# Kernel optimization log

Measured on AMD Instinct MI355X. Metric: run time of the kernel, lower is better.

The kernel has to match this reference:

```python
import jax, jax.numpy as jnp
import numpy as np

B, T, HID = 1, 2048, 2048
H = 16            # num_heads == num_key_value_heads
D = HID // H      # head_dim == feature_dim == 128
EPS = 1e-5


def _layer_norm(x, eps=1e-5):
    mu = jnp.mean(x, axis=-1, keepdims=True)
    var = jnp.mean((x - mu) ** 2, axis=-1, keepdims=True)
    return (x - mu) * jax.lax.rsqrt(var + eps)


def _feature_map(x, gamma, beta):
    # ReBased feature map, flatten=False (parallel mode): affine then LayerNorm
    return _layer_norm(x * gamma + beta)


def setup_inputs() -> dict:
    key = jax.random.key(0)
    ks = jax.random.split(key, 8)
    s = HID ** -0.5
    return {
        "hidden_states": jax.random.normal(ks[0], (B, T, HID), jnp.float32),
        "Wq": jax.random.normal(ks[1], (HID, HID), jnp.float32) * s,
        "Wk": jax.random.normal(ks[2], (HID, HID), jnp.float32) * s,
        "Wv": jax.random.normal(ks[3], (HID, HID), jnp.float32) * s,
        "Wo": jax.random.normal(ks[4], (HID, HID), jnp.float32) * s,
        "gamma": 1.0 + 0.1 * jax.random.normal(ks[5], (D,), jnp.float32),
        "beta": 0.1 * jax.random.normal(ks[6], (D,), jnp.float32),
    }


def reference(hidden_states, Wq, Wk, Wv, Wo, gamma, beta):
    b, t, _ = hidden_states.shape
    # projections (nn.Linear: x @ W.T), split into heads: [b, t, h, d]
    q = (hidden_states @ Wq.T).reshape(b, t, H, D)
    k = (hidden_states @ Wk.T).reshape(b, t, H, D)
    v = (hidden_states @ Wv.T).reshape(b, t, H, D)
    # ReBased feature map (no quadratic flatten in parallel mode)
    q = _feature_map(q, gamma, beta)
    k = _feature_map(k, gamma, beta)
    # parallel_rebased: scale q, quadratic score, causal mask, normalize
    q = q * (D ** -0.5)
    attn = jnp.einsum('bqhd,bkhd->bhqk', q, k) ** 2  # (q.k)^2
    mask = jnp.tril(jnp.ones((t, t), dtype=bool))
    attn = jnp.where(mask, attn, 0.0)
    o = jnp.einsum('bhqk,bkhd->bqhd', attn, v)       # [b, t, h, d]
    z = jnp.sum(attn, axis=-1)                       # [b, h, t]
    o = o / (jnp.swapaxes(z, 1, 2)[..., None] + EPS)
    o = o.reshape(b, t, H * D)
    return o @ Wo.T
```

## Files before the change

kernel.cpp:

```cpp
#include <hip/hip_runtime.h>
#include <hip/hip_bf16.h>
#include <stdint.h>

typedef __bf16 bf16;
typedef __bf16 v8bf __attribute__((ext_vector_type(8)));
typedef __bf16 v4bf __attribute__((ext_vector_type(4)));
typedef float  v4f  __attribute__((ext_vector_type(4)));

#define TSEQ   2048
#define HIDDIM 2048
#define NHEAD  16
#define HDIM   128

__device__ __forceinline__ void async16(void* lds, const void* g)
{
    __builtin_amdgcn_global_load_lds(
        (__attribute__((address_space(1))) void*)(uintptr_t)g,
        (__attribute__((address_space(3))) void*)(unsigned int)(uintptr_t)lds,
        16, 0, 0);
}

__global__ __launch_bounds__(256) void conv5(const float* __restrict__ s0, bf16* __restrict__ d0,
                                             const float* __restrict__ s1, bf16* __restrict__ d1,
                                             const float* __restrict__ s2, bf16* __restrict__ d2,
                                             const float* __restrict__ s3, bf16* __restrict__ d3,
                                             const float* __restrict__ s4, bf16* __restrict__ d4)
{
    const float* src; bf16* dst;
    switch (blockIdx.y) {
        case 0: src = s0; dst = d0; break;
        case 1: src = s1; dst = d1; break;
        case 2: src = s2; dst = d2; break;
        case 3: src = s3; dst = d3; break;
        default: src = s4; dst = d4; break;
    }
    const size_t i = ((size_t)blockIdx.x * 256 + threadIdx.x) * 8;
    const float4 a = *(const float4*)(src + i);
    const float4 b = *(const float4*)(src + i + 4);
    v8bf o;
    o[0] = (bf16)a.x; o[1] = (bf16)a.y; o[2] = (bf16)a.z; o[3] = (bf16)a.w;
    o[4] = (bf16)b.x; o[5] = (bf16)b.y; o[6] = (bf16)b.z; o[7] = (bf16)b.w;
    *(v8bf*)(dst + i) = o;
}


#define PBAR() do { __builtin_amdgcn_sched_barrier(0); __builtin_amdgcn_s_barrier(); \
                    __builtin_amdgcn_sched_barrier(0); } while (0)

#define STU(ldst, gsrc) do { \
    async16((ldst) + w*512,        (gsrc) + (size_t)(w*8 + (l>>3))*2048); \
    async16((ldst) + 4096 + w*512, (gsrc) + (size_t)(64 + w*8 + (l>>3))*2048); \
} while (0)

#define RDA(buf) do { _Pragma("unroll") \
    for (int mi_ = 0; mi_ < 4; ++mi_) { \
        const bf16* p_ = &sA[(buf)*8192 + (wm*64 + mi_*16 + lr)*64]; \
        a[mi_][0] = *(const v8bf*)(p_ + c0); \
        a[mi_][1] = *(const v8bf*)(p_ + c1); } } while (0)

#define RDB(buf, nh) do { _Pragma("unroll") \
    for (int nj_ = 0; nj_ < 2; ++nj_) { \
        const bf16* p_ = &sB[(buf)*24576 + ((nh)*128 + wn*32 + nj_*16 + lr)*64]; \
        b[nj_][0] = *(const v8bf*)(p_ + c0); \
        b[nj_][1] = *(const v8bf*)(p_ + c1); } } while (0)

#define MQ(nh) do { _Pragma("unroll") \
    for (int mi_ = 0; mi_ < 4; ++mi_) { _Pragma("unroll") \
        for (int nj_ = 0; nj_ < 2; ++nj_) { \
            acc[mi_][(nh)*2+nj_] = __builtin_amdgcn_mfma_f32_16x16x32_bf16( \
                a[mi_][0], b[nj_][0], acc[mi_][(nh)*2+nj_], 0, 0, 0); \
            acc[mi_][(nh)*2+nj_] = __builtin_amdgcn_mfma_f32_16x16x32_bf16( \
                a[mi_][1], b[nj_][1], acc[mi_][(nh)*2+nj_], 0, 0, 0); \
        } } } while (0)

#define VMC(n) asm volatile("s_waitcnt vmcnt(" #n ")" ::: "memory")

__global__ __launch_bounds__(512, 2) void gemm_qkv384(const bf16* __restrict__ A,
    const bf16* __restrict__ Wcat, bf16* __restrict__ qb, bf16* __restrict__ kb,
    bf16* __restrict__ vt, const float* __restrict__ gamma, const float* __restrict__ beta)
{
    __shared__ __attribute__((aligned(16))) bf16 sA[2*8192];
    __shared__ __attribute__((aligned(16))) bf16 sB[2*24576];
    const int n0g = blockIdx.x * 384;
    const int m0  = blockIdx.y * 128;

    const int tid = threadIdx.x, l = tid & 63, w = tid >> 6;
    const int wm = w >> 2, wn = w & 3;
    const int quad = l >> 4, lr = l & 15;
    const int scol = ((l & 7) ^ ((l >> 3) & 7)) * 8;
    const int c0 = ((quad    ) ^ (lr & 7)) * 8;
    const int c1 = ((quad + 4) ^ (lr & 7)) * 8;

    const bf16* Ag = A    + (size_t)m0  * 2048 + scol;
    const bf16* Bg = Wcat + (size_t)n0g * 2048 + scol;

    v4f  acc[4][6] = {};
    v8bf a[4][2], b[2][2];

    STU(&sA[0],           Ag);
    STU(&sB[0],           Bg);
    STU(&sB[8192],        Bg + (size_t)128*2048);
    STU(&sB[16384],       Bg + (size_t)256*2048);
    STU(&sA[8192],        Ag + 64);
    STU(&sB[24576],       Bg + 64);
    STU(&sB[24576+8192],  Bg + (size_t)128*2048 + 64);
    VMC(10);
    __builtin_amdgcn_s_barrier();
    __builtin_amdgcn_sched_barrier(0);

#pragma unroll 1
    for (int it = 0; it < 16; ++it) {
        const int k1 =  it*128 + 64;
        const int k2 = (it*128 + 128) & 2047;
        const int k3 = (it*128 + 192) & 2047;

        RDA(0); RDB(0, 0);
        STU(&sB[24576+16384], Bg + (size_t)256*2048 + k1);
        PBAR(); __builtin_amdgcn_s_setprio(1); MQ(0); __builtin_amdgcn_s_setprio(0);
        VMC(10); PBAR();
        RDB(0, 1);
        STU(&sA[0], Ag + k2);
        STU(&sB[0], Bg + k2);
        PBAR(); __builtin_amdgcn_s_setprio(1); MQ(1); __builtin_amdgcn_s_setprio(0);
        VMC(12); PBAR();
        RDB(0, 2);
        STU(&sB[8192], Bg + (size_t)128*2048 + k2);
        PBAR(); __builtin_amdgcn_s_setprio(1); MQ(2); __builtin_amdgcn_s_setprio(0);
        VMC(10); PBAR();
        RDA(1); RDB(1, 0);
        STU(&sB[16384], Bg + (size_t)256*2048 + k2);
        PBAR(); __builtin_amdgcn_s_setprio(1); MQ(0); __builtin_amdgcn_s_setprio(0);
        VMC(10); PBAR();
        RDB(1, 1);
        STU(&sA[8192],  Ag + k3);
        STU(&sB[24576], Bg + k3);
        PBAR(); __builtin_amdgcn_s_setprio(1); MQ(1); __builtin_amdgcn_s_setprio(0);
        VMC(12); PBAR();
        RDB(1, 2);
        STU(&sB[24576+8192], Bg + (size_t)128*2048 + k3);
        PBAR(); __builtin_amdgcn_s_setprio(1); MQ(2); __builtin_amdgcn_s_setprio(0);
        VMC(10); PBAR();
    }
    VMC(0);
    __syncthreads();

    bf16* sT = sB;
    const int erow = tid >> 2;
    const int ecol = (tid & 3) * 32;
    float gv[32], bv[32];
#pragma unroll
    for (int i = 0; i < 8; ++i) {
        *(float4*)&gv[i*4] = *(const float4*)(gamma + ecol + i*4);
        *(float4*)&bv[i*4] = *(const float4*)(beta  + ecol + i*4);
    }

#pragma unroll
    for (int nh = 0; nh < 3; ++nh) {
        const int colg0 = n0g + nh*128;
        const int which = colg0 >> 11;
        if (which == 2) {
#pragma unroll
            for (int mi = 0; mi < 4; ++mi) {
                const int row = m0 + wm*64 + mi*16 + quad*4;
#pragma unroll
                for (int jj = 0; jj < 2; ++jj) {
                    const int c = (colg0 & 2047) + wn*32 + jj*16 + lr;
                    v4bf pk;
#pragma unroll
                    for (int r = 0; r < 4; ++r) pk[r] = (bf16)acc[mi][nh*2+jj][r];
                    *(v4bf*)(vt + (size_t)c*2048 + row) = pk;
                }
            }
        } else {
#pragma unroll
            for (int mi = 0; mi < 4; ++mi) {
                const int row = wm*64 + mi*16 + quad*4;
#pragma unroll
                for (int jj = 0; jj < 2; ++jj) {
                    const int col = wn*32 + jj*16 + lr;
#pragma unroll
                    for (int r = 0; r < 4; ++r)
                        sT[(row + r)*136 + col] = (bf16)acc[mi][nh*2+jj][r];
                }
            }
            __syncthreads();
            float x[32];
            float s = 0.f, q = 0.f;
#pragma unroll
            for (int i = 0; i < 4; ++i) {
                const v8bf v = *(const v8bf*)&sT[erow*136 + ecol + i*8];
#pragma unroll
                for (int k = 0; k < 8; ++k) {
                    const float xv = (float)v[k] * gv[i*8+k] + bv[i*8+k];
                    x[i*8+k] = xv; s += xv; q += xv*xv;
                }
            }
            s += __shfl_xor(s, 1); q += __shfl_xor(q, 1);
            s += __shfl_xor(s, 2); q += __shfl_xor(q, 2);
            const float mu = s * (1.0f/128.0f);
            float var = q * (1.0f/128.0f) - mu*mu;
            var = fmaxf(var, 0.0f);
            bf16* Cb = (which == 0) ? qb : kb;
            const float qs = (which == 0) ? 0.08838834764831845f : 1.0f;
            const float rstd = rsqrtf(var + 1e-5f) * qs;
            bf16* dst = Cb + (size_t)(m0 + erow)*2048 + (colg0 & 2047) + ecol;
#pragma unroll
            for (int i = 0; i < 4; ++i) {
                v8bf o;
#pragma unroll
                for (int k = 0; k < 8; ++k)
                    o[k] = (bf16)((x[i*8+k] - mu) * rstd);
                *(v8bf*)(dst + i*8) = o;
            }
            __syncthreads();
        }
    }
}


#define RDO(aa, bb, buf) do { _Pragma("unroll") \
    for (int mi_ = 0; mi_ < 4; ++mi_) { \
        const bf16* p_ = &sA[(buf)*8192 + (wm*64 + mi_*16 + lr)*64]; \
        aa[mi_][0] = *(const v8bf*)(p_ + c0); \
        aa[mi_][1] = *(const v8bf*)(p_ + c1); } \
    _Pragma("unroll") \
    for (int nj_ = 0; nj_ < 2; ++nj_) { \
        const bf16* p_ = &sB[(buf)*8192 + (wn*32 + nj_*16 + lr)*64]; \
        bb[nj_][0] = *(const v8bf*)(p_ + c0); \
        bb[nj_][1] = *(const v8bf*)(p_ + c1); } } while (0)

#define MQO(aa, bb) do { _Pragma("unroll") \
    for (int mi_ = 0; mi_ < 4; ++mi_) { _Pragma("unroll") \
        for (int nj_ = 0; nj_ < 2; ++nj_) { \
            acc[mi_][nj_] = __builtin_amdgcn_mfma_f32_16x16x32_bf16( \
                aa[mi_][0], bb[nj_][0], acc[mi_][nj_], 0, 0, 0); \
            acc[mi_][nj_] = __builtin_amdgcn_mfma_f32_16x16x32_bf16( \
                aa[mi_][1], bb[nj_][1], acc[mi_][nj_], 0, 0, 0); \
        } } } while (0)

__global__ __launch_bounds__(512, 2) void gemm_out(const bf16* __restrict__ A,
    const bf16* __restrict__ B, float* __restrict__ C)
{
    __shared__ __attribute__((aligned(16))) bf16 sA[4*8192];
    __shared__ __attribute__((aligned(16))) bf16 sB[4*8192];
    const int m0 = blockIdx.y * 128, n0 = blockIdx.x * 128;
    const int tid = threadIdx.x, l = tid & 63, w = tid >> 6;
    const int wm = w >> 2, wn = w & 3;
    const int quad = l >> 4, lr = l & 15;
    const int scol = ((l & 7) ^ ((l >> 3) & 7)) * 8;
    const int c0 = ((quad    ) ^ (lr & 7)) * 8;
    const int c1 = ((quad + 4) ^ (lr & 7)) * 8;

    const bf16* Ag = A + (size_t)m0 * 2048 + scol;
    const bf16* Bg = B + (size_t)n0 * 2048 + scol;

    v4f  acc[4][2] = {};
    v8bf a0[4][2], b0[2][2], a1[4][2], b1[2][2];

    STU(&sA[0],    Ag);      STU(&sB[0],    Bg);
    STU(&sA[8192], Ag + 64); STU(&sB[8192], Bg + 64);
    VMC(0);
    __builtin_amdgcn_s_barrier();
    __builtin_amdgcn_sched_barrier(0);

#pragma unroll 2
    for (int p = 0; p < 16; ++p) {
        const int e = (p & 1) * 2;
        const int o = 2 - e;
        const int ks0 = ((2*p + 2) & 31) * 64;
        const int ks1 = ((2*p + 3) & 31) * 64;
        RDO(a0, b0, e);
        RDO(a1, b1, e + 1);
        STU(&sA[o*8192],       Ag + ks0);  STU(&sB[o*8192],       Bg + ks0);
        STU(&sA[(o+1)*8192],   Ag + ks1);  STU(&sB[(o+1)*8192],   Bg + ks1);
        PBAR();
        __builtin_amdgcn_s_setprio(1);
        MQO(a0, b0);
        MQO(a1, b1);
        __builtin_amdgcn_s_setprio(0);
        VMC(0);
        PBAR();
    }

#pragma unroll
    for (int mi = 0; mi < 4; ++mi) {
        const int row = m0 + wm*64 + mi*16 + quad*4;
#pragma unroll
        for (int nj = 0; nj < 2; ++nj) {
            const int col = n0 + wn*32 + nj*16 + lr;
#pragma unroll
            for (int r = 0; r < 4; ++r)
                C[(size_t)(row + r)*HIDDIM + col] = acc[mi][nj][r];
        }
    }
}

__global__ __launch_bounds__(512, 2) void attn(const bf16* __restrict__ qb,
                                               const bf16* __restrict__ kb,
                                               const bf16* __restrict__ vt,
                                               bf16* __restrict__ ob)
{
    __shared__ __attribute__((aligned(16))) bf16 sK[2*64*136];
    __shared__ __attribute__((aligned(16))) bf16 sV[2*128*72];
    __shared__ __attribute__((aligned(16))) bf16 sS[2*64*72];
    __shared__ __attribute__((aligned(16))) float sO[64*129];
    __shared__ __attribute__((aligned(16))) float sZ[64*17];

    const int h    = blockIdx.y;
    const int pr   = blockIdx.x;
    const int tid  = threadIdx.x, lane = tid & 63;
    const int w    = tid >> 6;
    const int g    = w >> 2;
    const int ww   = w & 3;
    const int quad = lane >> 4, lr = lane & 15;
    const int rs   = tid >> 4;
    const int cs   = (tid & 15) * 8;

#pragma unroll
    for (int ti = 0; ti < 2; ++ti) {
        const int tile = ti ? pr : (31 - pr);
        const int nch  = tile + 1;

        v8bf qa[4];
        {
            const bf16* q0 = qb + (size_t)(tile*64 + ww*16 + lr)*HIDDIM + h*HDIM + quad*8;
#pragma unroll
            for (int ks = 0; ks < 4; ++ks)
                qa[ks] = *(const v8bf*)(q0 + ks*32);
        }

        v4f  o[8] = {};
        float z[4] = {0.f, 0.f, 0.f, 0.f};

        v8bf curK[4], curV[4], nxtK[4], nxtV[4];
#pragma unroll
        for (int p = 0; p < 4; ++p) {
            curK[p] = *(const v8bf*)(kb + (size_t)(rs + p*32)*HIDDIM + h*HDIM + cs);
            curV[p] = *(const v8bf*)(vt + (size_t)(h*HDIM + rs + p*32)*HIDDIM + cs);
        }

        for (int ich = 0; ich < nch; ich += 2) {
            __syncthreads();
#pragma unroll
            for (int p = 0; p < 4; ++p) {
                const int r = rs + p*32;
                *(v8bf*)&sK[(r>>6)*8704 + (r&63)*136 + cs] = curK[p];
            }
#pragma unroll
            for (int p = 0; p < 4; ++p)
                *(v8bf*)&sV[(cs>>6)*9216 + (rs + p*32)*72 + (cs & 63)] = curV[p];

            if (ich + 2 < nch) {
                const int s1 = (ich + 2) * 64;
#pragma unroll
                for (int p = 0; p < 4; ++p) {
                    nxtK[p] = *(const v8bf*)(kb + (size_t)(s1 + rs + p*32)*HIDDIM + h*HDIM + cs);
                    nxtV[p] = *(const v8bf*)(vt + (size_t)(h*HDIM + rs + p*32)*HIDDIM + s1 + cs);
                }
            }
            __syncthreads();

            const int ch = ich + g;
            if (ch < nch) {
                const bf16* sKg = &sK[g*8704];
                const bf16* sVg = &sV[g*9216];
                bf16*       sSg = &sS[g*4608];
                const bool  diag = (ch == tile);
                const int   s0   = ch * 64;

                v8bf kbf[4][4];
#pragma unroll
                for (int nj = 0; nj < 4; ++nj)
#pragma unroll
                    for (int ks = 0; ks < 4; ++ks)
                        kbf[nj][ks] = *(const v8bf*)&sKg[(nj*16 + lr)*136 + ks*32 + quad*8];
                const int row_l = ww*16 + quad*4;
                const int qg    = tile*64 + row_l;
#pragma unroll
                for (int nj = 0; nj < 4; ++nj) {
                    v4f s4 = {0.f, 0.f, 0.f, 0.f};
#pragma unroll
                    for (int ks = 0; ks < 4; ++ks)
                        s4 = __builtin_amdgcn_mfma_f32_16x16x32_bf16(qa[ks], kbf[nj][ks], s4, 0, 0, 0);
                    const int col = nj*16 + lr;
                    const int sg  = s0 + col;
#pragma unroll
                    for (int r = 0; r < 4; ++r) {
                        float val = s4[r] * s4[r];
                        if (diag && (sg > qg + r)) val = 0.0f;
                        const bf16 vb16 = (bf16)val;
                        z[r] += (float)vb16;
                        sSg[(row_l + r)*72 + col] = vb16;
                    }
                }

#pragma unroll
                for (int ks = 0; ks < 2; ++ks) {
                    const v8bf sa = *(const v8bf*)&sSg[(ww*16 + lr)*72 + ks*32 + quad*8];
#pragma unroll
                    for (int nd = 0; nd < 8; ++nd) {
                        const v8bf vbf = *(const v8bf*)&sVg[(nd*16 + lr)*72 + ks*32 + quad*8];
                        o[nd] = __builtin_amdgcn_mfma_f32_16x16x32_bf16(sa, vbf, o[nd], 0, 0, 0);
                    }
                }
            }

            if (ich + 2 < nch) {
#pragma unroll
                for (int p = 0; p < 4; ++p) { curK[p] = nxtK[p]; curV[p] = nxtV[p]; }
            }
        }

        const int row_l = ww*16 + quad*4;
        __syncthreads();
        if (g == 1) {
#pragma unroll
            for (int nd = 0; nd < 8; ++nd)
#pragma unroll
                for (int r = 0; r < 4; ++r)
                    sO[(row_l + r)*129 + nd*16 + lr] = o[nd][r];
#pragma unroll
            for (int r = 0; r < 4; ++r)
                sZ[(row_l + r)*17 + lr] = z[r];
        }
        __syncthreads();
        if (g == 0) {
#pragma unroll
            for (int nd = 0; nd < 8; ++nd)
#pragma unroll
                for (int r = 0; r < 4; ++r)
                    o[nd][r] += sO[(row_l + r)*129 + nd*16 + lr];
#pragma unroll
            for (int r = 0; r < 4; ++r) {
                float zz = z[r] + sZ[(row_l + r)*17 + lr];
                zz += __shfl_xor(zz, 1); zz += __shfl_xor(zz, 2);
                zz += __shfl_xor(zz, 4); zz += __shfl_xor(zz, 8);
                z[r] = zz + 1e-5f;
            }
            const size_t rbase = (size_t)(tile*64 + row_l)*HIDDIM + h*HDIM;
#pragma unroll
            for (int nd = 0; nd < 8; ++nd) {
                const int col = nd*16 + lr;
#pragma unroll
                for (int r = 0; r < 4; ++r)
                    ob[rbase + (size_t)r*HIDDIM + col] = (bf16)(o[nd][r] / z[r]);
            }
        }
    }
}

extern "C" void kernel_launch(void* const* d_in, const int* in_sizes, int n_in,
                              void* d_out, int out_size, void* d_ws, size_t ws_size,
                              hipStream_t stream)
{
    const float* hs    = (const float*)d_in[0];
    const float* Wq    = (const float*)d_in[1];
    const float* Wk    = (const float*)d_in[2];
    const float* Wv    = (const float*)d_in[3];
    const float* Wo    = (const float*)d_in[4];
    const float* gamma = (const float*)d_in[5];
    const float* beta  = (const float*)d_in[6];
    float* outp = (float*)d_out;

    const size_t MAT = (size_t)TSEQ * HIDDIM;

    bf16* ws   = (bf16*)d_ws;
    bf16* hs_b = ws + 0*MAT;
    bf16* ob   = hs_b;
    bf16* Wq_b = ws + 1*MAT;
    bf16* Wk_b = ws + 2*MAT;
    bf16* Wv_b = ws + 3*MAT;
    bf16* Wo_b = ws + 4*MAT;
    bf16* vt   = ws + 5*MAT;
    bf16* qb   = (bf16*)d_out;
    bf16* kb   = (bf16*)d_out + MAT;

    conv5<<<dim3(2048, 5), 256, 0, stream>>>(hs, hs_b, Wq, Wq_b, Wk, Wk_b, Wv, Wv_b, Wo, Wo_b);
    gemm_qkv384<<<dim3(16, 16), 512, 0, stream>>>(hs_b, Wq_b, qb, kb, vt, gamma, beta);
    attn<<<dim3(16, 16), 512, 0, stream>>>(qb, kb, vt, ob);
    gemm_out<<<dim3(16, 16), 512, 0, stream>>>(ob, Wo_b, outp);
}
```

Measured before the change: 246.4 us.

## Retile attention warps as 2x2 grid over query and key/value dims

Within each group, the four warps are reassigned from one 16-row query strip each to a 2x2 grid. Each warp now handles 32 query rows by 32 key columns for the score step and 32 rows by 64 output dims for the PV step, so each LDS fragment load feeds more MFMAs. Because a warp's score tile is now read by other warps, an extra block barrier is added between the score and PV phases. Partial z sums are reduced with shuffles and combined through shared memory as four partials per row.

```diff
diff --git a/kernel.cpp b/kernel.cpp
--- a/kernel.cpp
+++ b/kernel.cpp
@@ -217,7 +217,6 @@
     }
 }
 
-
 #define RDO(aa, bb, buf) do { _Pragma("unroll") \
     for (int mi_ = 0; mi_ < 4; ++mi_) { \
         const bf16* p_ = &sA[(buf)*8192 + (wm*64 + mi_*16 + lr)*64]; \
@@ -304,7 +303,7 @@
     __shared__ __attribute__((aligned(16))) bf16 sV[2*128*72];
     __shared__ __attribute__((aligned(16))) bf16 sS[2*64*72];
     __shared__ __attribute__((aligned(16))) float sO[64*129];
-    __shared__ __attribute__((aligned(16))) float sZ[64*17];
+    __shared__ __attribute__((aligned(16))) float sZ[64*20];
 
     const int h    = blockIdx.y;
     const int pr   = blockIdx.x;
@@ -312,6 +311,8 @@
     const int w    = tid >> 6;
     const int g    = w >> 2;
     const int ww   = w & 3;
+    const int wq   = ww >> 1;
+    const int wk   = ww & 1;
     const int quad = lane >> 4, lr = lane & 15;
     const int rs   = tid >> 4;
     const int cs   = (tid & 15) * 8;
@@ -321,16 +322,17 @@
         const int tile = ti ? pr : (31 - pr);
         const int nch  = tile + 1;
 
-        v8bf qa[4];
-        {
-            const bf16* q0 = qb + (size_t)(tile*64 + ww*16 + lr)*HIDDIM + h*HDIM + quad*8;
+        v8bf qa[2][4];
+#pragma unroll
+        for (int mi = 0; mi < 2; ++mi) {
+            const bf16* q0 = qb + (size_t)(tile*64 + wq*32 + mi*16 + lr)*HIDDIM + h*HDIM + quad*8;
 #pragma unroll
             for (int ks = 0; ks < 4; ++ks)
-                qa[ks] = *(const v8bf*)(q0 + ks*32);
-        }
-
-        v4f  o[8] = {};
-        float z[4] = {0.f, 0.f, 0.f, 0.f};
+                qa[mi][ks] = *(const v8bf*)(q0 + ks*32);
+        }
+
+        v4f  o[2][4] = {};
+        float z[2][4] = {};
 
         v8bf curK[4], curV[4], nxtK[4], nxtV[4];
 #pragma unroll
@@ -360,47 +362,58 @@
             }
             __syncthreads();
 
-            const int ch = ich + g;
-            if (ch < nch) {
-                const bf16* sKg = &sK[g*8704];
-                const bf16* sVg = &sV[g*9216];
-                bf16*       sSg = &sS[g*4608];
-                const bool  diag = (ch == tile);
-                const int   s0   = ch * 64;
-
-                v8bf kbf[4][4];
-#pragma unroll
-                for (int nj = 0; nj < 4; ++nj)
+            const int ch  = ich + g;
+            const bool act = (ch < nch);
+            const bf16* sKg = &sK[g*8704];
+            const bf16* sVg = &sV[g*9216];
+            bf16*       sSg = &sS[g*4608];
+
+            if (act) {
+                const bool diag = (ch == tile);
+                const int  s0   = ch * 64;
+                v8bf kbf[2][4];
+#pragma unroll
+                for (int nj = 0; nj < 2; ++nj)
 #pragma unroll
                     for (int ks = 0; ks < 4; ++ks)
-                        kbf[nj][ks] = *(const v8bf*)&sKg[(nj*16 + lr)*136 + ks*32 + quad*8];
-                const int row_l = ww*16 + quad*4;
-                const int qg    = tile*64 + row_l;
-#pragma unroll
-                for (int nj = 0; nj < 4; ++nj) {
-                    v4f s4 = {0.f, 0.f, 0.f, 0.f};
-#pragma unroll
-                    for (int ks = 0; ks < 4; ++ks)
-                        s4 = __builtin_amdgcn_mfma_f32_16x16x32_bf16(qa[ks], kbf[nj][ks], s4, 0, 0, 0);
-                    const int col = nj*16 + lr;
-                    const int sg  = s0 + col;
-#pragma unroll
-                    for (int r = 0; r < 4; ++r) {
-                        float val = s4[r] * s4[r];
-                        if (diag && (sg > qg + r)) val = 0.0f;
-                        const bf16 vb16 = (bf16)val;
-                        z[r] += (float)vb16;
-                        sSg[(row_l + r)*72 + col] = vb16;
+                        kbf[nj][ks] = *(const v8bf*)&sKg[(wk*32 + nj*16 + lr)*136 + ks*32 + quad*8];
+#pragma unroll
+                for (int mi = 0; mi < 2; ++mi) {
+                    const int qg = tile*64 + wq*32 + mi*16 + quad*4;
+#pragma unroll
+                    for (int nj = 0; nj < 2; ++nj) {
+                        v4f s4 = {0.f, 0.f, 0.f, 0.f};
+#pragma unroll
+                        for (int ks = 0; ks < 4; ++ks)
+                            s4 = __builtin_amdgcn_mfma_f32_16x16x32_bf16(qa[mi][ks], kbf[nj][ks], s4, 0, 0, 0);
+                        const int col = wk*32 + nj*16 + lr;
+                        const int sg  = s0 + col;
+#pragma unroll
+                        for (int r = 0; r < 4; ++r) {
+                            float val = s4[r] * s4[r];
+                            if (diag && (sg > qg + r)) val = 0.0f;
+                            const bf16 vb16 = (bf16)val;
+                            z[mi][r] += (float)vb16;
+                            sSg[(wq*32 + mi*16 + quad*4 + r)*72 + col] = vb16;
+                        }
                     }
                 }
-
+            }
+            __syncthreads();
+
+            if (act) {
 #pragma unroll
                 for (int ks = 0; ks < 2; ++ks) {
-                    const v8bf sa = *(const v8bf*)&sSg[(ww*16 + lr)*72 + ks*32 + quad*8];
-#pragma unroll
-                    for (int nd = 0; nd < 8; ++nd) {
-                        const v8bf vbf = *(const v8bf*)&sVg[(nd*16 + lr)*72 + ks*32 + quad*8];
-                        o[nd] = __builtin_amdgcn_mfma_f32_16x16x32_bf16(sa, vbf, o[nd], 0, 0, 0);
+                    v8bf sa[2];
+#pragma unroll
+                    for (int mi = 0; mi < 2; ++mi)
+                        sa[mi] = *(const v8bf*)&sSg[(wq*32 + mi*16 + lr)*72 + ks*32 + quad*8];
+#pragma unroll
+                    for (int nd = 0; nd < 4; ++nd) {
+                        const v8bf vbf = *(const v8bf*)&sVg[(wk*64 + nd*16 + lr)*72 + ks*32 + quad*8];
+#pragma unroll
+                        for (int mi = 0; mi < 2; ++mi)
+                            o[mi][nd] = __builtin_amdgcn_mfma_f32_16x16x32_bf16(sa[mi], vbf, o[mi][nd], 0, 0, 0);
                     }
                 }
             }
@@ -411,39 +424,48 @@
             }
         }
 
-        const int row_l = ww*16 + quad*4;
-        __syncthreads();
+#pragma unroll
+        for (int mi = 0; mi < 2; ++mi)
+#pragma unroll
+            for (int r = 0; r < 4; ++r) {
+                float zz = z[mi][r];
+                zz += __shfl_xor(zz, 1); zz += __shfl_xor(zz, 2);
+                zz += __shfl_xor(zz, 4); zz += __shfl_xor(zz, 8);
+                if (lr == 0)
+                    sZ[(wq*32 + mi*16 + quad*4 + r)*20 + g*2 + wk] = zz;
+            }
         if (g == 1) {
 #pragma unroll
-            for (int nd = 0; nd < 8; ++nd)
-#pragma unroll
-                for (int r = 0; r < 4; ++r)
-                    sO[(row_l + r)*129 + nd*16 + lr] = o[nd][r];
-#pragma unroll
-            for (int r = 0; r < 4; ++r)
-                sZ[(row_l + r)*17 + lr] = z[r];
+            for (int mi = 0; mi < 2; ++mi)
+#pragma unroll
+                for (int nd = 0; nd < 4; ++nd)
+#pragma unroll
+                    for (int r = 0; r < 4; ++r)
+                        sO[(wq*32 + mi*16 + quad*4 + r)*129 + wk*64 + nd*16 + lr] = o[mi][nd][r];
         }
         __syncthreads();
         if (g == 0) {
-#pragma unroll
-            for (int nd = 0; nd < 8; ++nd)
-#pragma unroll
-                for (int r = 0; r < 4; ++r)
-                    o[nd][r] += sO[(row_l + r)*129 + nd*16 + lr];
-#pragma unroll
-            for (int r = 0; r < 4; ++r) {
-                float zz = z[r] + sZ[(row_l + r)*17 + lr];
-                zz += __shfl_xor(zz, 1); zz += __shfl_xor(zz, 2);
-                zz += __shfl_xor(zz, 4); zz += __shfl_xor(zz, 8);
-                z[r] = zz + 1e-5f;
-            }
-            const size_t rbase = (size_t)(tile*64 + row_l)*HIDDIM + h*HDIM;
-#pragma unroll
-            for (int nd = 0; nd < 8; ++nd) {
-                const int col = nd*16 + lr;
-#pragma unroll
-                for (int r = 0; r < 4; ++r)
-                    ob[rbase + (size_t)r*HIDDIM + col] = (bf16)(o[nd][r] / z[r]);
+            float zv[2][4];
+#pragma unroll
+            for (int mi = 0; mi < 2; ++mi)
+#pragma unroll
+                for (int r = 0; r < 4; ++r) {
+                    const float4 zp = *(const float4*)&sZ[(wq*32 + mi*16 + quad*4 + r)*20];
+                    zv[mi][r] = zp.x + zp.y + zp.z + zp.w + 1e-5f;
+                }
+#pragma unroll
+            for (int mi = 0; mi < 2; ++mi) {
+                const int row_l = wq*32 + mi*16 + quad*4;
+                const size_t rbase = (size_t)(tile*64 + row_l)*HIDDIM + h*HDIM;
+#pragma unroll
+                for (int nd = 0; nd < 4; ++nd) {
+                    const int col = wk*64 + nd*16 + lr;
+#pragma unroll
+                    for (int r = 0; r < 4; ++r) {
+                        const float ov = o[mi][nd][r] + sO[(row_l + r)*129 + col];
+                        ob[rbase + (size_t)r*HIDDIM + col] = (bf16)(ov / zv[mi][r]);
+                    }
+                }
             }
         }
     }
```

After: 249.8 us. Within noise of the previous version (+1.4%).

## Fuse Wo fp32-to-bf16 conversion into output GEMM B-tile loading

Applied to the files above, without the earlier changes.

Drops Wo from the standalone conversion kernel and instead has gemm_out load fp32 Wo tiles into registers, convert them to bf16 and write them into LDS inside the pipelined loop. This removes one 16 MB fp32 read plus an 8 MB bf16 write and reread through the workspace. In exchange each gemm_out block reads fp32 B tiles (twice the bytes, fetched repeatedly across the 16 M-blocks), and it uses register-staged loads instead of async LDS loads, which raises register pressure and may hurt overlap.

```diff
diff --git a/kernel.cpp b/kernel.cpp
--- a/kernel.cpp
+++ b/kernel.cpp
@@ -23,16 +23,14 @@
 __global__ __launch_bounds__(256) void conv5(const float* __restrict__ s0, bf16* __restrict__ d0,
                                              const float* __restrict__ s1, bf16* __restrict__ d1,
                                              const float* __restrict__ s2, bf16* __restrict__ d2,
-                                             const float* __restrict__ s3, bf16* __restrict__ d3,
-                                             const float* __restrict__ s4, bf16* __restrict__ d4)
+                                             const float* __restrict__ s3, bf16* __restrict__ d3)
 {
     const float* src; bf16* dst;
     switch (blockIdx.y) {
         case 0: src = s0; dst = d0; break;
         case 1: src = s1; dst = d1; break;
         case 2: src = s2; dst = d2; break;
-        case 3: src = s3; dst = d3; break;
-        default: src = s4; dst = d4; break;
+        default: src = s3; dst = d3; break;
     }
     const size_t i = ((size_t)blockIdx.x * 256 + threadIdx.x) * 8;
     const float4 a = *(const float4*)(src + i);
@@ -217,7 +215,6 @@
     }
 }
 
-
 #define RDO(aa, bb, buf) do { _Pragma("unroll") \
     for (int mi_ = 0; mi_ < 4; ++mi_) { \
         const bf16* p_ = &sA[(buf)*8192 + (wm*64 + mi_*16 + lr)*64]; \
@@ -238,8 +235,23 @@
                 aa[mi_][1], bb[nj_][1], acc[mi_][nj_], 0, 0, 0); \
         } } } while (0)
 
+#define LDBF(fbuf, gsrcf) do { _Pragma("unroll") \
+    for (int u_ = 0; u_ < 2; ++u_) { \
+        const float* sp_ = (gsrcf) + (size_t)(u_*64 + w*8 + (l>>3))*2048 + scol; \
+        fbuf[u_][0] = *(const float4*)(sp_); \
+        fbuf[u_][1] = *(const float4*)(sp_ + 4); } } while (0)
+
+#define WRBF(ldst, fbuf) do { _Pragma("unroll") \
+    for (int u_ = 0; u_ < 2; ++u_) { \
+        v8bf t_; \
+        t_[0] = (bf16)fbuf[u_][0].x; t_[1] = (bf16)fbuf[u_][0].y; \
+        t_[2] = (bf16)fbuf[u_][0].z; t_[3] = (bf16)fbuf[u_][0].w; \
+        t_[4] = (bf16)fbuf[u_][1].x; t_[5] = (bf16)fbuf[u_][1].y; \
+        t_[6] = (bf16)fbuf[u_][1].z; t_[7] = (bf16)fbuf[u_][1].w; \
+        *(v8bf*)((ldst) + u_*4096 + w*512 + l*8) = t_; } } while (0)
+
 __global__ __launch_bounds__(512, 2) void gemm_out(const bf16* __restrict__ A,
-    const bf16* __restrict__ B, float* __restrict__ C)
+    const float* __restrict__ Bf, float* __restrict__ C)
 {
     __shared__ __attribute__((aligned(16))) bf16 sA[4*8192];
     __shared__ __attribute__((aligned(16))) bf16 sB[4*8192];
@@ -251,17 +263,19 @@
     const int c0 = ((quad    ) ^ (lr & 7)) * 8;
     const int c1 = ((quad + 4) ^ (lr & 7)) * 8;
 
-    const bf16* Ag = A + (size_t)m0 * 2048 + scol;
-    const bf16* Bg = B + (size_t)n0 * 2048 + scol;
+    const bf16*  Ag = A  + (size_t)m0 * 2048 + scol;
+    const float* Bg = Bf + (size_t)n0 * 2048;
 
     v4f  acc[4][2] = {};
     v8bf a0[4][2], b0[2][2], a1[4][2], b1[2][2];
-
-    STU(&sA[0],    Ag);      STU(&sB[0],    Bg);
-    STU(&sA[8192], Ag + 64); STU(&sB[8192], Bg + 64);
+    float4 fb0[2][2], fb1[2][2];
+
+    LDBF(fb0, Bg); LDBF(fb1, Bg + 64);
+    STU(&sA[0],    Ag);
+    STU(&sA[8192], Ag + 64);
     VMC(0);
-    __builtin_amdgcn_s_barrier();
-    __builtin_amdgcn_sched_barrier(0);
+    WRBF(&sB[0], fb0); WRBF(&sB[8192], fb1);
+    __syncthreads();
 
 #pragma unroll 2
     for (int p = 0; p < 16; ++p) {
@@ -269,16 +283,20 @@
         const int o = 2 - e;
         const int ks0 = ((2*p + 2) & 31) * 64;
         const int ks1 = ((2*p + 3) & 31) * 64;
+        LDBF(fb0, Bg + ks0);
+        LDBF(fb1, Bg + ks1);
         RDO(a0, b0, e);
         RDO(a1, b1, e + 1);
-        STU(&sA[o*8192],       Ag + ks0);  STU(&sB[o*8192],       Bg + ks0);
-        STU(&sA[(o+1)*8192],   Ag + ks1);  STU(&sB[(o+1)*8192],   Bg + ks1);
+        STU(&sA[o*8192],     Ag + ks0);
+        STU(&sA[(o+1)*8192], Ag + ks1);
         PBAR();
         __builtin_amdgcn_s_setprio(1);
         MQO(a0, b0);
         MQO(a1, b1);
         __builtin_amdgcn_s_setprio(0);
         VMC(0);
+        WRBF(&sB[o*8192],     fb0);
+        WRBF(&sB[(o+1)*8192], fb1);
         PBAR();
     }
 
@@ -470,13 +488,12 @@
     bf16* Wq_b = ws + 1*MAT;
     bf16* Wk_b = ws + 2*MAT;
     bf16* Wv_b = ws + 3*MAT;
-    bf16* Wo_b = ws + 4*MAT;
     bf16* vt   = ws + 5*MAT;
     bf16* qb   = (bf16*)d_out;
     bf16* kb   = (bf16*)d_out + MAT;
 
-    conv5<<<dim3(2048, 5), 256, 0, stream>>>(hs, hs_b, Wq, Wq_b, Wk, Wk_b, Wv, Wv_b, Wo, Wo_b);
+    conv5<<<dim3(2048, 4), 256, 0, stream>>>(hs, hs_b, Wq, Wq_b, Wk, Wk_b, Wv, Wv_b);
     gemm_qkv384<<<dim3(16, 16), 512, 0, stream>>>(hs_b, Wq_b, qb, kb, vt, gamma, beta);
     attn<<<dim3(16, 16), 512, 0, stream>>>(qb, kb, vt, ob);
-    gemm_out<<<dim3(16, 16), 512, 0, stream>>>(ob, Wo_b, outp);
-}
+    gemm_out<<<dim3(16, 16), 512, 0, stream>>>(ob, Wo, outp);
+}
```

After: 258.6 us. +5.0%, slower.
